# Performance work log

Hardware: AMD Instinct MI355X
Metric: run time of the kernel (lower is better)

## Reference

```python
import jax, jax.numpy as jnp
import numpy as np

DIM = 512
NUM_HEADS = 8
WS = 7
HEAD_DIM = DIM // NUM_HEADS
SCALE = HEAD_DIM ** -0.5
THETA = 10000.0


def _freqs_cis_2d(hd, end):
    # 2D axial RoPE: interleaved (x,y) complex rotations per frequency
    Hg = int(end ** 0.5)
    pos = jnp.arange(end)
    x_pos = (pos % Hg).astype(jnp.float32)
    y_pos = (pos // Hg).astype(jnp.float32)
    freqs = 1.0 / THETA ** (jnp.arange(0, hd, 4)[: hd // 4].astype(jnp.float32) / hd)
    x_cis = jnp.exp(1j * jnp.outer(x_pos, freqs))  # (end, hd//4) complex64
    y_cis = jnp.exp(1j * jnp.outer(y_pos, freqs))
    return jnp.stack([x_cis, y_cis], axis=-1).reshape(end, -1)  # (end, hd//2)


def setup_inputs() -> dict:
    key = jax.random.key(0)
    k1, k2, k3 = jax.random.split(key, 3)
    B, H, W, C = 32, 56, 56, DIM
    x = jax.random.normal(k1, (B, H * W, C), dtype=jnp.float32)
    w_qkv = jax.random.normal(k2, (3 * C, C), dtype=jnp.float32) * 0.02
    w_proj = jax.random.normal(k3, (C, C), dtype=jnp.float32) * 0.02
    b_proj = jnp.zeros((C,), dtype=jnp.float32)
    return {"x": x, "w_qkv": w_qkv, "w_proj": w_proj, "b_proj": b_proj, "H": H, "W": W}


def reference(x, w_qkv, w_proj, b_proj, H, W):
    B, N, C = x.shape
    nh, hd, ws = NUM_HEADS, HEAD_DIM, WS
    _h, _w = H // ws, W // ws
    G, S = _h * _w, ws * ws
    # window partition: (B, _h, _w, ws, ws, C)
    xw = x.reshape(B, _h, ws, _w, ws, C).transpose(0, 1, 3, 2, 4, 5)
    qkv = jnp.einsum('bhwpqc,dc->bhwpqd', xw, w_qkv).reshape(B, G, S, 3, nh, hd)
    q, k, v = qkv[..., 0, :, :], qkv[..., 1, :, :], qkv[..., 2, :, :]  # (B,G,S,nh,hd)

    fc = _freqs_cis_2d(hd, S)  # (S, hd//2) complex64

    def rope(t):
        tc = t.reshape(*t.shape[:-1], hd // 2, 2)
        tc = jax.lax.complex(tc[..., 0], tc[..., 1])       # (B,G,S,nh,hd//2)
        tc = tc * fc[None, None, :, None, :]
        return jnp.stack([tc.real, tc.imag], axis=-1).reshape(t.shape)

    q = rope(q)
    k = rope(k)
    attn = jnp.einsum('bgsnd,bgtnd->bgnst', q, k) * SCALE  # (B,G,nh,S,S)
    attn = jax.nn.softmax(attn, axis=-1)
    out = jnp.einsum('bgnst,bgtnd->bgsnd', attn, v)        # (B,G,S,nh,hd)
    # window merge back to (B, H, W, C)
    out = out.reshape(B, _h, _w, ws, ws, C).transpose(0, 1, 3, 2, 4, 5).reshape(B, N, C)
    return jnp.einsum('bnc,dc->bnd', out, w_proj) + b_proj
```

## Files before the change

kernel.cpp:

```cpp
#include <hip/hip_runtime.h>
#include <stdint.h>
#include <stddef.h>

typedef _Float16 f16;
typedef _Float16 f16x8 __attribute__((ext_vector_type(8)));
typedef _Float16 f16x4 __attribute__((ext_vector_type(4)));
typedef float    f32x4 __attribute__((ext_vector_type(4)));

#define AS1 __attribute__((address_space(1)))
#define AS3 __attribute__((address_space(3)))

__device__ __forceinline__ void gl_lds16(const f16* g, f16* l) {
  __builtin_amdgcn_global_load_lds((const AS1 uint32_t*)g, (AS3 uint32_t*)l, 16, 0, 0);
}


__global__ __launch_bounds__(256) void k_prep(
    const float* __restrict__ x, const float* __restrict__ wqkv,
    const float* __restrict__ wproj,
    f16* __restrict__ x16, f16* __restrict__ wqkv16, f16* __restrict__ wproj16,
    float2* __restrict__ tab)
{
  const int XB = 25088, WQ = 384, WP = 128;
  int b = blockIdx.x, t = threadIdx.x;
  const float* src; f16* dst; long i0;
  if (b < XB)            { src = x;     dst = x16;     i0 = ((long)b*256 + t)*8; }
  else if (b < XB+WQ)    { src = wqkv;  dst = wqkv16;  i0 = ((long)(b-XB)*256 + t)*8; }
  else if (b < XB+WQ+WP) { src = wproj; dst = wproj16; i0 = ((long)(b-XB-WQ)*256 + t)*8; }
  else {
    int id = (b - XB - WQ - WP)*256 + t;
    if (id < 49*32) {
      int s = id >> 5, i = id & 31, j = i >> 1;
      float freq = expf(-(float)(4*j)*(1.0f/64.0f)*9.210340372f);
      float pos = (i & 1) ? (float)(s/7) : (float)(s%7);
      float a = pos * freq;
      tab[id] = make_float2(cosf(a), sinf(a));
    }
    return;
  }
  const float4* s4 = (const float4*)(src + i0);
  float4 v0 = s4[0], v1 = s4[1];
  f16x8 h = { (f16)v0.x,(f16)v0.y,(f16)v0.z,(f16)v0.w,
              (f16)v1.x,(f16)v1.y,(f16)v1.z,(f16)v1.w };
  *(f16x8*)(dst + i0) = h;
}

__global__ __launch_bounds__(256) void k_qkv(
    const f16* __restrict__ x16, const f16* __restrict__ w16,
    const float2* __restrict__ tab,
    f16* __restrict__ qb, f16* __restrict__ kb, f16* __restrict__ vb)
{
  __shared__ __align__(16) f16 Wt[128*32];
  __shared__ __align__(16) f16 Xt[128*32];
  const int by = blockIdx.x;
  const int bx = blockIdx.y;
  const int tid = threadIdx.x;
  const int wave = tid >> 6, ln = tid & 63;
  const int l15 = ln & 15, quad = ln >> 4;
  const int wq = wave >> 1, wp = wave & 1;

  f32x4 acc[4][4] = {};

  const int srow = wave*32 + (ln >> 2);
  const int scol = (ln & 3)*8;
  const f16* gW = w16 + (size_t)(by*128 + srow)*512 + scol;
  const f16* gX = x16 + (size_t)(bx*128 + srow)*512 + scol;
  f16* lW = &Wt[srow*32 + scol];
  f16* lX = &Xt[srow*32 + scol];

  for (int kt = 0; kt < 16; ++kt) {
    __syncthreads();
    gl_lds16(gW,          lW);
    gl_lds16(gW + 16*512, lW + 16*32);
    gl_lds16(gX,          lX);
    gl_lds16(gX + 16*512, lX + 16*32);
    gW += 32; gX += 32;
    __syncthreads();
    f16x8 af[4], bf[4];
#pragma unroll
    for (int i = 0; i < 4; ++i) af[i] = *(const f16x8*)&Wt[(wq*64 + i*16 + l15)*32 + quad*8];
#pragma unroll
    for (int j = 0; j < 4; ++j) bf[j] = *(const f16x8*)&Xt[(wp*64 + j*16 + l15)*32 + quad*8];
#pragma unroll
    for (int i = 0; i < 4; ++i)
#pragma unroll
      for (int j = 0; j < 4; ++j)
        acc[i][j] = __builtin_amdgcn_mfma_f32_16x16x32_f16(af[i], bf[j], acc[i][j], 0, 0, 0);
  }

  const int t = (by*128) >> 9;
#pragma unroll
  for (int j = 0; j < 4; ++j) {
    int m  = bx*128 + wp*64 + j*16 + l15;
    int b  = m / 3136;
    int nn = m - b*3136;
    int hh = nn / 56, ww = nn - hh*56;
    int gh = hh / 7,  p  = hh - gh*7;
    int gw = ww / 7,  qx = ww - gw*7;
    int g  = gh*8 + gw;
    int s  = p*7 + qx;
    int bg = b*64 + g;
#pragma unroll
    for (int i = 0; i < 4; ++i) {
      int c0   = by*128 + wq*64 + i*16 + quad*4;
      int cin  = c0 & 511;
      int head = cin >> 6;
      int dd   = cin & 63;
      float v0 = acc[i][j][0], v1 = acc[i][j][1], v2 = acc[i][j][2], v3 = acc[i][j][3];
      if (t < 2) {
        float2 t0 = tab[s*32 + (dd >> 1)];
        float2 t1 = tab[s*32 + (dd >> 1) + 1];
        float r0 = v0*t0.x - v1*t0.y;
        float r1 = v0*t0.y + v1*t0.x;
        float r2 = v2*t1.x - v3*t1.y;
        float r3 = v2*t1.y + v3*t1.x;
        f16x4 h4 = { (f16)r0, (f16)r1, (f16)r2, (f16)r3 };
        f16* dst = (t == 0 ? qb : kb) + (size_t)((bg*8 + head)*49 + s)*64 + dd;
        *(f16x4*)dst = h4;
      } else {
        size_t base = (size_t)((bg*8 + head)*64 + dd)*56 + s;
        vb[base      ] = (f16)v0;
        vb[base +  56] = (f16)v1;
        vb[base + 112] = (f16)v2;
        vb[base + 168] = (f16)v3;
      }
    }
  }
}

__global__ __launch_bounds__(64) void k_attn(
    const f16* __restrict__ qb, const f16* __restrict__ kb,
    const f16* __restrict__ vb, f16* __restrict__ ob)
{
  __shared__ __align__(16) f16 P[64*72];
  __shared__ float lsum[64];
  const int bid = blockIdx.x;
  const int ln = threadIdx.x, l15 = ln & 15, quad = ln >> 4;
  const f16* q = qb + (size_t)bid*(49*64);
  const f16* k = kb + (size_t)bid*(49*64);
  const f16* v = vb + (size_t)bid*(64*56);

  f32x4 a[4][4] = {};
#pragma unroll
  for (int kt = 0; kt < 2; ++kt) {
    f16x8 qf[4], kf[4];
#pragma unroll
    for (int mt = 0; mt < 4; ++mt) {
      int s = mt*16 + l15; if (s > 48) s = 48;
      qf[mt] = *(const f16x8*)(q + s*64 + kt*32 + quad*8);
      kf[mt] = *(const f16x8*)(k + s*64 + kt*32 + quad*8);
    }
#pragma unroll
    for (int mt = 0; mt < 4; ++mt)
#pragma unroll
      for (int nt = 0; nt < 4; ++nt)
        a[mt][nt] = __builtin_amdgcn_mfma_f32_16x16x32_f16(qf[mt], kf[nt], a[mt][nt], 0, 0, 0);
  }

  const float scale = 0.125f;
#pragma unroll
  for (int mt = 0; mt < 4; ++mt) {
    float mx[4] = {-1e30f,-1e30f,-1e30f,-1e30f};
#pragma unroll
    for (int nt = 0; nt < 4; ++nt) {
      int col = nt*16 + l15;
      bool valid = col < 49;
#pragma unroll
      for (int r = 0; r < 4; ++r) {
        float vv = valid ? a[mt][nt][r]*scale : -1e30f;
        a[mt][nt][r] = vv;
        mx[r] = fmaxf(mx[r], vv);
      }
    }
#pragma unroll
    for (int d = 1; d < 16; d <<= 1)
#pragma unroll
      for (int r = 0; r < 4; ++r) mx[r] = fmaxf(mx[r], __shfl_xor(mx[r], d, 64));
    float sm[4] = {0.f,0.f,0.f,0.f};
#pragma unroll
    for (int nt = 0; nt < 4; ++nt)
#pragma unroll
      for (int r = 0; r < 4; ++r) {
        float e = __expf(a[mt][nt][r] - mx[r]);
        a[mt][nt][r] = e;
        sm[r] += e;
      }
#pragma unroll
    for (int d = 1; d < 16; d <<= 1)
#pragma unroll
      for (int r = 0; r < 4; ++r) sm[r] += __shfl_xor(sm[r], d, 64);
#pragma unroll
    for (int nt = 0; nt < 4; ++nt)
#pragma unroll
      for (int r = 0; r < 4; ++r)
        P[(mt*16 + quad*4 + r)*72 + nt*16 + l15] = (f16)a[mt][nt][r];
    if (l15 == 0) {
#pragma unroll
      for (int r = 0; r < 4; ++r) lsum[mt*16 + quad*4 + r] = sm[r];
    }
  }
  __syncthreads();

  f32x4 o[4][4] = {};
#pragma unroll
  for (int kt = 0; kt < 2; ++kt) {
    int s0 = kt*32 + quad*8; if (s0 >= 56) s0 = 40;
    f16x8 vf[4], pf[4];
#pragma unroll
    for (int dt = 0; dt < 4; ++dt) vf[dt] = *(const f16x8*)(v + (dt*16 + l15)*56 + s0);
#pragma unroll
    for (int st = 0; st < 4; ++st) pf[st] = *(const f16x8*)&P[(st*16 + l15)*72 + kt*32 + quad*8];
#pragma unroll
    for (int dt = 0; dt < 4; ++dt)
#pragma unroll
      for (int st = 0; st < 4; ++st)
        o[dt][st] = __builtin_amdgcn_mfma_f32_16x16x32_f16(vf[dt], pf[st], o[dt][st], 0, 0, 0);
  }

  const int bg = bid >> 3, head = bid & 7;
#pragma unroll
  for (int st = 0; st < 4; ++st) {
    int sq = st*16 + l15;
    if (sq < 49) {
      float inv = 1.0f / lsum[sq];
#pragma unroll
      for (int dt = 0; dt < 4; ++dt) {
        int d0 = dt*16 + quad*4;
        f16x4 h4 = { (f16)(o[dt][st][0]*inv), (f16)(o[dt][st][1]*inv),
                     (f16)(o[dt][st][2]*inv), (f16)(o[dt][st][3]*inv) };
        *(f16x4*)(ob + (size_t)(bg*49 + sq)*512 + head*64 + d0) = h4;
      }
    }
  }
}

__global__ __launch_bounds__(256) void k_proj(
    const f16* __restrict__ a16, const f16* __restrict__ w16,
    const float* __restrict__ bias, float* __restrict__ out)
{
  __shared__ __align__(16) f16 Wt[128*32];
  __shared__ __align__(16) f16 Xt[128*32];
  const int by = blockIdx.x;
  const int bx = blockIdx.y;
  const int tid = threadIdx.x;
  const int wave = tid >> 6, ln = tid & 63;
  const int l15 = ln & 15, quad = ln >> 4;
  const int wq = wave >> 1, wp = wave & 1;

  f32x4 acc[4][4] = {};

  const int srow = wave*32 + (ln >> 2);
  const int scol = (ln & 3)*8;
  const f16* gW = w16 + (size_t)(by*128 + srow)*512 + scol;
  const f16* gX = a16 + (size_t)(bx*128 + srow)*512 + scol;
  f16* lW = &Wt[srow*32 + scol];
  f16* lX = &Xt[srow*32 + scol];

  for (int kt = 0; kt < 16; ++kt) {
    __syncthreads();
    gl_lds16(gW,          lW);
    gl_lds16(gW + 16*512, lW + 16*32);
    gl_lds16(gX,          lX);
    gl_lds16(gX + 16*512, lX + 16*32);
    gW += 32; gX += 32;
    __syncthreads();
    f16x8 af[4], bf[4];
#pragma unroll
    for (int i = 0; i < 4; ++i) af[i] = *(const f16x8*)&Wt[(wq*64 + i*16 + l15)*32 + quad*8];
#pragma unroll
    for (int j = 0; j < 4; ++j) bf[j] = *(const f16x8*)&Xt[(wp*64 + j*16 + l15)*32 + quad*8];
#pragma unroll
    for (int i = 0; i < 4; ++i)
#pragma unroll
      for (int j = 0; j < 4; ++j)
        acc[i][j] = __builtin_amdgcn_mfma_f32_16x16x32_f16(af[i], bf[j], acc[i][j], 0, 0, 0);
  }

#pragma unroll
  for (int j = 0; j < 4; ++j) {
    int m  = bx*128 + wp*64 + j*16 + l15;
    int b  = m / 3136;
    int rr = m - b*3136;
    int g  = rr / 49;
    int s  = rr - g*49;
    int gh = g >> 3, gw = g & 7;
    int p  = s / 7,  qx = s - p*7;
    int hh = gh*7 + p, ww = gw*7 + qx;
    size_t tok = (size_t)b*3136 + hh*56 + ww;
#pragma unroll
    for (int i = 0; i < 4; ++i) {
      int d0 = by*128 + wq*64 + i*16 + quad*4;
      float4 bb = *(const float4*)(bias + d0);
      float4 o4 = make_float4(acc[i][j][0]+bb.x, acc[i][j][1]+bb.y,
                              acc[i][j][2]+bb.z, acc[i][j][3]+bb.w);
      *(float4*)(out + tok*512 + d0) = o4;
    }
  }
}

extern "C" void kernel_launch(void* const* d_in, const int* in_sizes, int n_in,
                              void* d_out, int out_size, void* d_ws, size_t ws_size,
                              hipStream_t stream) {
  const float* x     = (const float*)d_in[0];
  const float* wqkv  = (const float*)d_in[1];
  const float* wproj = (const float*)d_in[2];
  const float* bias  = (const float*)d_in[3];

  char* ws = (char*)d_ws;
  f16*    x16   = (f16*)(ws);
  f16*    wq16  = (f16*)(ws + 102760448);
  f16*    wp16  = (f16*)(ws + 104333312);
  float2* tab   = (float2*)(ws + 104857600);
  f16*    vT    = (f16*)(ws + 104873984);
  f16*    attn16 = (f16*)(ws);

  f16* qbuf = (f16*)d_out;
  f16* kbuf = (f16*)((char*)d_out + 102760448);
  float* out = (float*)d_out;

  k_prep<<<dim3(25088 + 384 + 128 + 7), dim3(256), 0, stream>>>(
      x, wqkv, wproj, x16, wq16, wp16, tab);
  k_qkv<<<dim3(12, 784), dim3(256), 0, stream>>>(x16, wq16, tab, qbuf, kbuf, vT);
  k_attn<<<dim3(16384), dim3(64), 0, stream>>>(qbuf, kbuf, vT, attn16);
  k_proj<<<dim3(4, 784), dim3(256), 0, stream>>>(attn16, wp16, bias, out);
}
```

Before: 957.4 us.

## Deepen GEMM K-tile with XOR-swizzled LDS and store V row-major

```diff
diff --git a/kernel.cpp b/kernel.cpp
--- a/kernel.cpp
+++ b/kernel.cpp
@@ -45,13 +45,45 @@
   *(f16x8*)(dst + i0) = h;
 }
 
+#define GEMM_STAGE(gW, gX, Wt, Xt, kt)                                        \
+  {                                                                           \
+    int srow = ln >> 3;                        \
+    int schunk = (ln & 7) ^ srow;              \
+    size_t goff = (size_t)srow * 512 + (kt)*64 + schunk * 8;                  \
+    _Pragma("unroll")                                                         \
+    for (int ii = 0; ii < 4; ++ii) {                                          \
+      int r0 = wave * 32 + ii * 8;                                            \
+      gl_lds16(gW + (size_t)r0 * 512 + goff, Wt + r0 * 64);                   \
+      gl_lds16(gX + (size_t)r0 * 512 + goff, Xt + r0 * 64);                   \
+    }                                                                         \
+  }
+
+#define GEMM_MAIN(Wt, Xt)                                                     \
+  _Pragma("unroll")                                                           \
+  for (int k2 = 0; k2 < 2; ++k2) {                                            \
+    f16x8 af[4], bf[4];                                                       \
+    int pc = ((k2 * 4 + quad) ^ (l15 & 7)) * 8;                               \
+    _Pragma("unroll")                                                         \
+    for (int i = 0; i < 4; ++i)                                               \
+      af[i] = *(const f16x8*)&Wt[(wq * 64 + i * 16 + l15) * 64 + pc];         \
+    _Pragma("unroll")                                                         \
+    for (int j = 0; j < 4; ++j)                                               \
+      bf[j] = *(const f16x8*)&Xt[(wp * 64 + j * 16 + l15) * 64 + pc];         \
+    _Pragma("unroll")                                                         \
+    for (int i = 0; i < 4; ++i)                                               \
+      _Pragma("unroll")                                                       \
+      for (int j = 0; j < 4; ++j)                                             \
+        acc[i][j] = __builtin_amdgcn_mfma_f32_16x16x32_f16(af[i], bf[j],      \
+                                                           acc[i][j], 0, 0, 0);\
+  }
+
 __global__ __launch_bounds__(256) void k_qkv(
     const f16* __restrict__ x16, const f16* __restrict__ w16,
     const float2* __restrict__ tab,
     f16* __restrict__ qb, f16* __restrict__ kb, f16* __restrict__ vb)
 {
-  __shared__ __align__(16) f16 Wt[128*32];
-  __shared__ __align__(16) f16 Xt[128*32];
+  __shared__ __align__(16) f16 Wt[128*64];
+  __shared__ __align__(16) f16 Xt[128*64];
   const int by = blockIdx.x;
   const int bx = blockIdx.y;
   const int tid = threadIdx.x;
@@ -60,32 +92,14 @@
   const int wq = wave >> 1, wp = wave & 1;
 
   f32x4 acc[4][4] = {};
-
-  const int srow = wave*32 + (ln >> 2);
-  const int scol = (ln & 3)*8;
-  const f16* gW = w16 + (size_t)(by*128 + srow)*512 + scol;
-  const f16* gX = x16 + (size_t)(bx*128 + srow)*512 + scol;
-  f16* lW = &Wt[srow*32 + scol];
-  f16* lX = &Xt[srow*32 + scol];
-
-  for (int kt = 0; kt < 16; ++kt) {
+  const f16* gW = w16 + (size_t)(by*128)*512;
+  const f16* gX = x16 + (size_t)(bx*128)*512;
+
+  for (int kt = 0; kt < 8; ++kt) {
     __syncthreads();
-    gl_lds16(gW,          lW);
-    gl_lds16(gW + 16*512, lW + 16*32);
-    gl_lds16(gX,          lX);
-    gl_lds16(gX + 16*512, lX + 16*32);
-    gW += 32; gX += 32;
+    GEMM_STAGE(gW, gX, Wt, Xt, kt);
     __syncthreads();
-    f16x8 af[4], bf[4];
-#pragma unroll
-    for (int i = 0; i < 4; ++i) af[i] = *(const f16x8*)&Wt[(wq*64 + i*16 + l15)*32 + quad*8];
-#pragma unroll
-    for (int j = 0; j < 4; ++j) bf[j] = *(const f16x8*)&Xt[(wp*64 + j*16 + l15)*32 + quad*8];
-#pragma unroll
-    for (int i = 0; i < 4; ++i)
-#pragma unroll
-      for (int j = 0; j < 4; ++j)
-        acc[i][j] = __builtin_amdgcn_mfma_f32_16x16x32_f16(af[i], bf[j], acc[i][j], 0, 0, 0);
+    GEMM_MAIN(Wt, Xt);
   }
 
   const int t = (by*128) >> 9;
@@ -107,23 +121,20 @@
       int head = cin >> 6;
       int dd   = cin & 63;
       float v0 = acc[i][j][0], v1 = acc[i][j][1], v2 = acc[i][j][2], v3 = acc[i][j][3];
+      f16x4 h4;
       if (t < 2) {
         float2 t0 = tab[s*32 + (dd >> 1)];
         float2 t1 = tab[s*32 + (dd >> 1) + 1];
-        float r0 = v0*t0.x - v1*t0.y;
-        float r1 = v0*t0.y + v1*t0.x;
-        float r2 = v2*t1.x - v3*t1.y;
-        float r3 = v2*t1.y + v3*t1.x;
-        f16x4 h4 = { (f16)r0, (f16)r1, (f16)r2, (f16)r3 };
-        f16* dst = (t == 0 ? qb : kb) + (size_t)((bg*8 + head)*49 + s)*64 + dd;
-        *(f16x4*)dst = h4;
+        h4[0] = (f16)(v0*t0.x - v1*t0.y);
+        h4[1] = (f16)(v0*t0.y + v1*t0.x);
+        h4[2] = (f16)(v2*t1.x - v3*t1.y);
+        h4[3] = (f16)(v2*t1.y + v3*t1.x);
       } else {
-        size_t base = (size_t)((bg*8 + head)*64 + dd)*56 + s;
-        vb[base      ] = (f16)v0;
-        vb[base +  56] = (f16)v1;
-        vb[base + 112] = (f16)v2;
-        vb[base + 168] = (f16)v3;
+        h4[0] = (f16)v0; h4[1] = (f16)v1; h4[2] = (f16)v2; h4[3] = (f16)v3;
       }
+      f16* dst = (t == 0 ? qb : (t == 1 ? kb : vb))
+               + (size_t)((bg*8 + head)*49 + s)*64 + dd;
+      *(f16x4*)dst = h4;
     }
   }
 }
@@ -132,13 +143,18 @@
     const f16* __restrict__ qb, const f16* __restrict__ kb,
     const f16* __restrict__ vb, f16* __restrict__ ob)
 {
+  __shared__ __align__(16) f16 Vt[64*64];
   __shared__ __align__(16) f16 P[64*72];
   __shared__ float lsum[64];
   const int bid = blockIdx.x;
   const int ln = threadIdx.x, l15 = ln & 15, quad = ln >> 4;
   const f16* q = qb + (size_t)bid*(49*64);
   const f16* k = kb + (size_t)bid*(49*64);
-  const f16* v = vb + (size_t)bid*(64*56);
+  const f16* v = vb + (size_t)bid*(49*64);
+
+#pragma unroll
+  for (int i = 0; i < 8; ++i)
+    gl_lds16(v + (size_t)(i*8 + (ln>>3))*64 + (ln&7)*8, Vt + i*512);
 
   f32x4 a[4][4] = {};
 #pragma unroll
@@ -204,12 +220,15 @@
   f32x4 o[4][4] = {};
 #pragma unroll
   for (int kt = 0; kt < 2; ++kt) {
-    int s0 = kt*32 + quad*8; if (s0 >= 56) s0 = 40;
+    const int s0 = kt*32 + quad*8;
     f16x8 vf[4], pf[4];
 #pragma unroll
-    for (int dt = 0; dt < 4; ++dt) vf[dt] = *(const f16x8*)(v + (dt*16 + l15)*56 + s0);
-#pragma unroll
-    for (int st = 0; st < 4; ++st) pf[st] = *(const f16x8*)&P[(st*16 + l15)*72 + kt*32 + quad*8];
+    for (int dt = 0; dt < 4; ++dt)
+#pragma unroll
+      for (int j = 0; j < 8; ++j)
+        vf[dt][j] = Vt[(s0 + j)*64 + dt*16 + l15];
+#pragma unroll
+    for (int st = 0; st < 4; ++st) pf[st] = *(const f16x8*)&P[(st*16 + l15)*72 + s0];
 #pragma unroll
     for (int dt = 0; dt < 4; ++dt)
 #pragma unroll
@@ -238,8 +257,8 @@
     const f16* __restrict__ a16, const f16* __restrict__ w16,
     const float* __restrict__ bias, float* __restrict__ out)
 {
-  __shared__ __align__(16) f16 Wt[128*32];
-  __shared__ __align__(16) f16 Xt[128*32];
+  __shared__ __align__(16) f16 Wt[128*64];
+  __shared__ __align__(16) f16 Xt[128*64];
   const int by = blockIdx.x;
   const int bx = blockIdx.y;
   const int tid = threadIdx.x;
@@ -248,32 +267,14 @@
   const int wq = wave >> 1, wp = wave & 1;
 
   f32x4 acc[4][4] = {};
-
-  const int srow = wave*32 + (ln >> 2);
-  const int scol = (ln & 3)*8;
-  const f16* gW = w16 + (size_t)(by*128 + srow)*512 + scol;
-  const f16* gX = a16 + (size_t)(bx*128 + srow)*512 + scol;
-  f16* lW = &Wt[srow*32 + scol];
-  f16* lX = &Xt[srow*32 + scol];
-
-  for (int kt = 0; kt < 16; ++kt) {
+  const f16* gW = w16 + (size_t)(by*128)*512;
+  const f16* gX = a16 + (size_t)(bx*128)*512;
+
+  for (int kt = 0; kt < 8; ++kt) {
     __syncthreads();
-    gl_lds16(gW,          lW);
-    gl_lds16(gW + 16*512, lW + 16*32);
-    gl_lds16(gX,          lX);
-    gl_lds16(gX + 16*512, lX + 16*32);
-    gW += 32; gX += 32;
+    GEMM_STAGE(gW, gX, Wt, Xt, kt);
     __syncthreads();
-    f16x8 af[4], bf[4];
-#pragma unroll
-    for (int i = 0; i < 4; ++i) af[i] = *(const f16x8*)&Wt[(wq*64 + i*16 + l15)*32 + quad*8];
-#pragma unroll
-    for (int j = 0; j < 4; ++j) bf[j] = *(const f16x8*)&Xt[(wp*64 + j*16 + l15)*32 + quad*8];
-#pragma unroll
-    for (int i = 0; i < 4; ++i)
-#pragma unroll
-      for (int j = 0; j < 4; ++j)
-        acc[i][j] = __builtin_amdgcn_mfma_f32_16x16x32_f16(af[i], bf[j], acc[i][j], 0, 0, 0);
+    GEMM_MAIN(Wt, Xt);
   }
 
 #pragma unroll
@@ -311,7 +312,7 @@
   f16*    wq16  = (f16*)(ws + 102760448);
   f16*    wp16  = (f16*)(ws + 104333312);
   float2* tab   = (float2*)(ws + 104857600);
-  f16*    vT    = (f16*)(ws + 104873984);
+  f16*    vbuf  = (f16*)(ws + 104873984);
   f16*    attn16 = (f16*)(ws);
 
   f16* qbuf = (f16*)d_out;
@@ -320,7 +321,7 @@
 
   k_prep<<<dim3(25088 + 384 + 128 + 7), dim3(256), 0, stream>>>(
       x, wqkv, wproj, x16, wq16, wp16, tab);
-  k_qkv<<<dim3(12, 784), dim3(256), 0, stream>>>(x16, wq16, tab, qbuf, kbuf, vT);
-  k_attn<<<dim3(16384), dim3(64), 0, stream>>>(qbuf, kbuf, vT, attn16);
+  k_qkv<<<dim3(12, 784), dim3(256), 0, stream>>>(x16, wq16, tab, qbuf, kbuf, vbuf);
+  k_attn<<<dim3(16384), dim3(64), 0, stream>>>(qbuf, kbuf, vbuf, attn16);
   k_proj<<<dim3(4, 784), dim3(256), 0, stream>>>(attn16, wp16, bias, out);
 }
```

New measurement: 889.7 us. -7.1%, faster.
